# Optimization experiments

Hardware: AMD Instinct MI355X
Metric: run time of the kernel (lower is better)

The kernel has to match this reference:

```python
import jax, jax.numpy as jnp
import numpy as np

B = 256          # batch
H = 1024         # conditioning_size (dec_hid_dim)
D = 256          # gst_dim
G = 32           # num_gst
C = 16           # num_cells
O = 256          # output_size


def setup_inputs() -> dict:
    key = jax.random.key(0)
    ks = jax.random.split(key, 7)
    hidden = jax.random.normal(ks[0], (B, H), dtype=jnp.float32)
    # per-cell embedding tables: nn.Embedding(num_gst, gst_dim) stacked over cells
    gst_emb = jax.random.normal(ks[1], (C, G, D), dtype=jnp.float32)
    # per-cell Linear(gst_dim + cond, cond): weight [H, H + D] (torch [out, in]), bias [H]
    attn_w = jax.random.normal(ks[2], (C, H, H + D), dtype=jnp.float32) * 0.02
    attn_b = jax.random.normal(ks[3], (C, H), dtype=jnp.float32) * 0.02
    # per-cell v: Parameter(torch.rand(cond))
    v = jax.random.uniform(ks[4], (C, H), dtype=jnp.float32)
    # out Linear(gst_dim, output_size)
    out_w = jax.random.normal(ks[5], (O, D), dtype=jnp.float32) * 0.02
    out_b = jax.random.normal(ks[6], (O,), dtype=jnp.float32) * 0.02
    return {"hidden": hidden, "gst_emb": gst_emb, "attn_w": attn_w,
            "attn_b": attn_b, "v": v, "out_w": out_w, "out_b": out_b}


def reference(hidden, gst_emb, attn_w, attn_b, v, out_w, out_b):
    # Original concatenates (hidden, encoder_outputs) along features; split the
    # linear weight accordingly instead of materializing the concat.
    w_hid = attn_w[:, :, :H]        # [C, H, H]
    w_enc = attn_w[:, :, H:]        # [C, H, D]
    # embedding lookup of arange(G) == the table rows themselves (same for all batch)
    enc = gst_emb                   # [C, G, D]
    hid_part = jnp.einsum('bh,coh->bco', hidden, w_hid)     # [B, C, Ho]
    enc_part = jnp.einsum('cgd,cod->cgo', enc, w_enc)       # [C, G, Ho]
    energy = jnp.tanh(hid_part[:, :, None, :] + enc_part[None]
                      + attn_b[None, :, None, :])           # [B, C, G, Ho]
    scores = jnp.einsum('bcgh,ch->bcg', energy, v)          # [B, C, G]
    attention = jax.nn.softmax(scores, axis=-1)             # softmax over num_gst
    weighted = jnp.einsum('bcg,cgd->bcd', attention, enc)   # [B, C, D]
    att_cat = attention.reshape(B, C * G)                   # torch.cat(att_list, dim=1)
    pooled = jnp.mean(weighted, axis=1)                     # [B, D]
    out = pooled @ out_w.T + out_b                          # [B, O]
    return (att_cat, out)
```

## Files before the change

kernel.cpp:

```cpp
#include <hip/hip_runtime.h>
#include <hip/hip_bf16.h>

#define B_  256
#define H_  1024
#define D_  256
#define G_  32
#define C_  16
#define O_  256
#define HD_ 1280
#define N1_ 16384
#define RS_ 36

typedef __attribute__((ext_vector_type(8))) short short8;
typedef __attribute__((ext_vector_type(4))) short s16x4;
typedef __attribute__((ext_vector_type(4))) float f32x4;

#define MFMA16(a, b, c) __builtin_amdgcn_mfma_f32_16x16x32_bf16((a), (b), (c), 0, 0, 0)

__device__ __forceinline__ float tanh_c(float x) {
    float y = __expf(2.f * x);
    float t = 1.f - 2.f * __builtin_amdgcn_rcpf(y + 1.f);
    return fminf(fmaxf(t, -0.99999994f), 0.99999994f);
}

__device__ __forceinline__ short bfhi(float x) {
    return (short)(__float_as_uint(x) >> 16);
}
__device__ __forceinline__ short bflo(float x) {
    float fhi = __uint_as_float(__float_as_uint(x) & 0xFFFF0000u);
    return (short)(__float_as_uint(x - fhi) >> 16);
}

__device__ __forceinline__ void split4(const float4 v, s16x4& hi, s16x4& lo) {
    hi[0] = bfhi(v.x); lo[0] = bflo(v.x);
    hi[1] = bfhi(v.y); lo[1] = bflo(v.y);
    hi[2] = bfhi(v.z); lo[2] = bflo(v.z);
    hi[3] = bfhi(v.w); lo[3] = bflo(v.w);
}

__global__ __launch_bounds__(512) void gemm1_kernel(
    const float* __restrict__ hidden, const float* __restrict__ attn_w,
    const float* __restrict__ attn_b, float* __restrict__ hp)
{
    __shared__ short AsH[128 * RS_];
    __shared__ short AsL[128 * RS_];
    __shared__ short BsH[64 * RS_];
    __shared__ short BsL[64 * RS_];

    const int tid  = threadIdx.x;
    const int wave = tid >> 6, lane = tid & 63;
    const int m0 = blockIdx.x * 128;
    const int n0 = blockIdx.y * 64;
    const int wm = (wave >> 1) * 32;
    const int wn = (wave & 1) * 32;
    const int l16 = lane & 15;
    const int lk  = (lane >> 4) * 8;

    f32x4 acc[2][2];
    for (int mi = 0; mi < 2; ++mi)
        for (int ni = 0; ni < 2; ++ni)
            acc[mi][ni] = f32x4{0.f, 0.f, 0.f, 0.f};

    int rA[2], cA[2];
    #pragma unroll
    for (int i = 0; i < 2; ++i) {
        const int chunk = tid + i * 512;
        rA[i] = chunk >> 3;
        cA[i] = (chunk & 7) * 4;
    }
    const int rB = tid >> 3, cB = (tid & 7) * 4;

    const float* pA0 = hidden + rA[0] * H_ + m0 * H_ + cA[0];
    const float* pA1 = hidden + rA[1] * H_ + m0 * H_ + cA[1];
    const float* pB  = attn_w + (size_t)(n0 + rB) * HD_ + cB;

    float4 va[2], vb;
    va[0] = *(const float4*)(pA0);
    va[1] = *(const float4*)(pA1);
    vb    = *(const float4*)(pB);

    for (int k0 = 0; k0 < H_; k0 += 32) {
        __syncthreads();
        #pragma unroll
        for (int i = 0; i < 2; ++i) {
            s16x4 h, l;
            split4(va[i], h, l);
            *(s16x4*)(AsH + rA[i] * RS_ + cA[i]) = h;
            *(s16x4*)(AsL + rA[i] * RS_ + cA[i]) = l;
        }
        {
            s16x4 h, l;
            split4(vb, h, l);
            *(s16x4*)(BsH + rB * RS_ + cB) = h;
            *(s16x4*)(BsL + rB * RS_ + cB) = l;
        }
        __syncthreads();

        if (k0 + 32 < H_) {
            const int kn = k0 + 32;
            va[0] = *(const float4*)(pA0 + kn);
            va[1] = *(const float4*)(pA1 + kn);
            vb    = *(const float4*)(pB  + kn);
        }

        short8 ah[2], al[2], bh[2], bl[2];
        #pragma unroll
        for (int mi = 0; mi < 2; ++mi) {
            ah[mi] = *(const short8*)(AsH + (wm + mi * 16 + l16) * RS_ + lk);
            al[mi] = *(const short8*)(AsL + (wm + mi * 16 + l16) * RS_ + lk);
        }
        #pragma unroll
        for (int ni = 0; ni < 2; ++ni) {
            bh[ni] = *(const short8*)(BsH + (wn + ni * 16 + l16) * RS_ + lk);
            bl[ni] = *(const short8*)(BsL + (wn + ni * 16 + l16) * RS_ + lk);
        }
        #pragma unroll
        for (int mi = 0; mi < 2; ++mi)
            #pragma unroll
            for (int ni = 0; ni < 2; ++ni) {
                acc[mi][ni] = MFMA16(ah[mi], bh[ni], acc[mi][ni]);
                acc[mi][ni] = MFMA16(al[mi], bh[ni], acc[mi][ni]);
                acc[mi][ni] = MFMA16(ah[mi], bl[ni], acc[mi][ni]);
            }
    }

    const int lr = (lane >> 4) * 4;
    #pragma unroll
    for (int mi = 0; mi < 2; ++mi) {
        #pragma unroll
        for (int ni = 0; ni < 2; ++ni) {
            const int col  = n0 + wn + ni * 16 + l16;
            const float bias = attn_b[col];
            float* dst = hp + (size_t)(m0 + wm + mi * 16 + lr) * N1_ + col;
            f32x4 vacc = acc[mi][ni];
            dst[0]        = tanh_c(vacc[0] + bias);
            dst[N1_]      = tanh_c(vacc[1] + bias);
            dst[2 * N1_]  = tanh_c(vacc[2] + bias);
            dst[3 * N1_]  = tanh_c(vacc[3] + bias);
        }
    }
}

__global__ __launch_bounds__(256) void gemm2_kernel(
    const float* __restrict__ enc, const float* __restrict__ attn_w,
    float* __restrict__ ep)
{
    const int tid  = threadIdx.x;
    const int wave = tid >> 6, lane = tid & 63;
    const int c  = blockIdx.y;
    const int n0 = blockIdx.x * 64 + wave * 16;
    const int l16 = lane & 15;
    const int lk  = (lane >> 4) * 8;

    f32x4 acc[2];
    acc[0] = f32x4{0.f, 0.f, 0.f, 0.f};
    acc[1] = f32x4{0.f, 0.f, 0.f, 0.f};

    const float* encp = enc + c * (G_ * D_);
    const float* wp   = attn_w + (size_t)c * H_ * HD_ + H_;

    #pragma unroll
    for (int kk = 0; kk < 8; ++kk) {
        const int k0 = kk * 32 + lk;
        short8 ah[2], al[2], bh, bl;
        #pragma unroll
        for (int mi = 0; mi < 2; ++mi) {
            const float* p = encp + (mi * 16 + l16) * D_ + k0;
            s16x4 h0, l0, h1, l1;
            split4(*(const float4*)p, h0, l0);
            split4(*(const float4*)(p + 4), h1, l1);
            ah[mi] = short8{h0[0],h0[1],h0[2],h0[3],h1[0],h1[1],h1[2],h1[3]};
            al[mi] = short8{l0[0],l0[1],l0[2],l0[3],l1[0],l1[1],l1[2],l1[3]};
        }
        {
            const float* p = wp + (size_t)(n0 + l16) * HD_ + k0;
            s16x4 h0, l0, h1, l1;
            split4(*(const float4*)p, h0, l0);
            split4(*(const float4*)(p + 4), h1, l1);
            bh = short8{h0[0],h0[1],h0[2],h0[3],h1[0],h1[1],h1[2],h1[3]};
            bl = short8{l0[0],l0[1],l0[2],l0[3],l1[0],l1[1],l1[2],l1[3]};
        }
        #pragma unroll
        for (int mi = 0; mi < 2; ++mi) {
            acc[mi] = MFMA16(ah[mi], bh, acc[mi]);
            acc[mi] = MFMA16(al[mi], bh, acc[mi]);
            acc[mi] = MFMA16(ah[mi], bl, acc[mi]);
        }
    }

    const int lr = (lane >> 4) * 4;
    #pragma unroll
    for (int mi = 0; mi < 2; ++mi) {
        const int g = mi * 16 + lr;
        const int o = n0 + l16;
        float* dst = ep + (c * G_ + g) * H_ + o;
        f32x4 vacc = acc[mi];
        dst[0]      = tanh_c(vacc[0]);
        dst[H_]     = tanh_c(vacc[1]);
        dst[2 * H_] = tanh_c(vacc[2]);
        dst[3 * H_] = tanh_c(vacc[3]);
    }
}

__global__ __launch_bounds__(256) void attn_kernel(
    const float* __restrict__ hp, const float* __restrict__ ep,
    const float* __restrict__ v, const float* __restrict__ enc,
    float* __restrict__ out, float* __restrict__ wt)
{
    const int c = blockIdx.x, b = blockIdx.y;
    const int tid  = threadIdx.x;
    const int wave = tid >> 6, lane = tid & 63;

    __shared__ float s_att[G_];
    __shared__ float s_sc[G_];

    float tav[16], vv[16];
    const float* hprow = hp + (size_t)b * N1_ + c * H_;
    const float* vrow  = v + c * H_;
    #pragma unroll
    for (int j = 0; j < 16; ++j) {
        const int o = lane + j * 64;
        tav[j] = hprow[o];
        vv[j]  = vrow[o];
    }

    #pragma unroll
    for (int gg = 0; gg < 8; ++gg) {
        const int g = wave * 8 + gg;
        const float* eprow = ep + (c * G_ + g) * H_;
        float s = 0.f;
        #pragma unroll
        for (int j = 0; j < 16; ++j) {
            const float tb  = eprow[lane + j * 64];
            const float ta  = tav[j];
            const float num = ta + tb;
            const float den = fmaf(ta, tb, 1.f);
            const float t   = num * __builtin_amdgcn_rcpf(den);
            s = fmaf(t, vv[j], s);
        }
        #pragma unroll
        for (int off = 32; off > 0; off >>= 1)
            s += __shfl_down(s, off, 64);
        if (lane == 0) s_sc[g] = s;
    }
    __syncthreads();

    if (tid < 32) {
        float s = s_sc[tid];
        float m = s;
        #pragma unroll
        for (int off = 16; off > 0; off >>= 1)
            m = fmaxf(m, __shfl_xor(m, off, 32));
        const float e = __expf(s - m);
        float sum = e;
        #pragma unroll
        for (int off = 16; off > 0; off >>= 1)
            sum += __shfl_xor(sum, off, 32);
        const float a = e / sum;
        s_att[tid] = a;
        out[(size_t)b * (C_ * G_) + c * G_ + tid] = a;
    }
    __syncthreads();

    float wsum = 0.f;
    const float* encc = enc + c * (G_ * D_) + tid;
    #pragma unroll
    for (int g = 0; g < G_; ++g)
        wsum += s_att[g] * encc[g * D_];
    wt[(size_t)(b * C_ + c) * D_ + tid] = wsum;
}

__global__ __launch_bounds__(256) void out_kernel(
    const float* __restrict__ wt, const float* __restrict__ out_w,
    const float* __restrict__ out_b, float* __restrict__ out)
{
    const int b = blockIdx.x, tid = threadIdx.x;
    __shared__ float pooled[D_];

    float s = 0.f;
    #pragma unroll
    for (int c = 0; c < C_; ++c)
        s += wt[(size_t)(b * C_ + c) * D_ + tid];
    pooled[tid] = s * (1.f / 16.f);
    __syncthreads();

    float acc = out_b[tid];
    const float* wrow = out_w + tid * D_;
    #pragma unroll 8
    for (int dc = 0; dc < 64; ++dc) {
        float4 w4 = *(const float4*)(wrow + dc * 4);
        acc += pooled[dc * 4 + 0] * w4.x;
        acc += pooled[dc * 4 + 1] * w4.y;
        acc += pooled[dc * 4 + 2] * w4.z;
        acc += pooled[dc * 4 + 3] * w4.w;
    }
    out[(size_t)B_ * (C_ * G_) + b * O_ + tid] = acc;
}

extern "C" void kernel_launch(void* const* d_in, const int* in_sizes, int n_in,
                              void* d_out, int out_size, void* d_ws, size_t ws_size,
                              hipStream_t stream) {
    const float* hidden = (const float*)d_in[0];
    const float* enc    = (const float*)d_in[1];
    const float* attn_w = (const float*)d_in[2];
    const float* attn_b = (const float*)d_in[3];
    const float* v      = (const float*)d_in[4];
    const float* out_w  = (const float*)d_in[5];
    const float* out_b  = (const float*)d_in[6];
    float* out = (float*)d_out;

    float* hp = (float*)d_ws;
    float* ep = hp + (size_t)B_ * N1_;
    float* wt = ep + (size_t)C_ * G_ * H_;

    gemm1_kernel<<<dim3(2, 256), 512, 0, stream>>>(hidden, attn_w, attn_b, hp);
    gemm2_kernel<<<dim3(16, C_), 256, 0, stream>>>(enc, attn_w, ep);
    attn_kernel<<<dim3(C_, B_), 256, 0, stream>>>(hp, ep, v, enc, out, wt);
    out_kernel<<<B_, 256, 0, stream>>>(wt, out_w, out_b, out);
}
```

Before: 207.7 us.

## Enlarge gemm1 tile to 128x128 and batch four rows per attention block

gemm1 now computes 128x128 output tiles, with each wave handling 64x32 instead of 32x32. This halves the grid and raises the MFMA work per LDS fragment load. The attention kernel processes four batch rows per block, so each ep row and enc element loaded is reused four times, and the grid shrinks by four. In exchange there is more register pressure (acc[4][2], tav[4][16]) and fewer blocks to spread across CUs.

```diff
diff --git a/kernel.cpp b/kernel.cpp
--- a/kernel.cpp
+++ b/kernel.cpp
@@ -44,40 +44,43 @@
 {
     __shared__ short AsH[128 * RS_];
     __shared__ short AsL[128 * RS_];
-    __shared__ short BsH[64 * RS_];
-    __shared__ short BsL[64 * RS_];
+    __shared__ short BsH[128 * RS_];
+    __shared__ short BsL[128 * RS_];
 
     const int tid  = threadIdx.x;
     const int wave = tid >> 6, lane = tid & 63;
     const int m0 = blockIdx.x * 128;
-    const int n0 = blockIdx.y * 64;
-    const int wm = (wave >> 1) * 32;
-    const int wn = (wave & 1) * 32;
+    const int n0 = blockIdx.y * 128;
+    const int wm = (wave >> 2) * 64;
+    const int wn = (wave & 3) * 32;
     const int l16 = lane & 15;
     const int lk  = (lane >> 4) * 8;
 
-    f32x4 acc[2][2];
-    for (int mi = 0; mi < 2; ++mi)
+    f32x4 acc[4][2];
+    #pragma unroll
+    for (int mi = 0; mi < 4; ++mi)
+        #pragma unroll
         for (int ni = 0; ni < 2; ++ni)
             acc[mi][ni] = f32x4{0.f, 0.f, 0.f, 0.f};
 
-    int rA[2], cA[2];
+    int rr[2], cc[2];
     #pragma unroll
     for (int i = 0; i < 2; ++i) {
         const int chunk = tid + i * 512;
-        rA[i] = chunk >> 3;
-        cA[i] = (chunk & 7) * 4;
-    }
-    const int rB = tid >> 3, cB = (tid & 7) * 4;
-
-    const float* pA0 = hidden + rA[0] * H_ + m0 * H_ + cA[0];
-    const float* pA1 = hidden + rA[1] * H_ + m0 * H_ + cA[1];
-    const float* pB  = attn_w + (size_t)(n0 + rB) * HD_ + cB;
-
-    float4 va[2], vb;
+        rr[i] = chunk >> 3;
+        cc[i] = (chunk & 7) * 4;
+    }
+
+    const float* pA0 = hidden + (m0 + rr[0]) * H_ + cc[0];
+    const float* pA1 = hidden + (m0 + rr[1]) * H_ + cc[1];
+    const float* pB0 = attn_w + (size_t)(n0 + rr[0]) * HD_ + cc[0];
+    const float* pB1 = attn_w + (size_t)(n0 + rr[1]) * HD_ + cc[1];
+
+    float4 va[2], vb[2];
     va[0] = *(const float4*)(pA0);
     va[1] = *(const float4*)(pA1);
-    vb    = *(const float4*)(pB);
+    vb[0] = *(const float4*)(pB0);
+    vb[1] = *(const float4*)(pB1);
 
     for (int k0 = 0; k0 < H_; k0 += 32) {
         __syncthreads();
@@ -85,14 +88,11 @@
         for (int i = 0; i < 2; ++i) {
             s16x4 h, l;
             split4(va[i], h, l);
-            *(s16x4*)(AsH + rA[i] * RS_ + cA[i]) = h;
-            *(s16x4*)(AsL + rA[i] * RS_ + cA[i]) = l;
-        }
-        {
-            s16x4 h, l;
-            split4(vb, h, l);
-            *(s16x4*)(BsH + rB * RS_ + cB) = h;
-            *(s16x4*)(BsL + rB * RS_ + cB) = l;
+            *(s16x4*)(AsH + rr[i] * RS_ + cc[i]) = h;
+            *(s16x4*)(AsL + rr[i] * RS_ + cc[i]) = l;
+            split4(vb[i], h, l);
+            *(s16x4*)(BsH + rr[i] * RS_ + cc[i]) = h;
+            *(s16x4*)(BsL + rr[i] * RS_ + cc[i]) = l;
         }
         __syncthreads();
 
@@ -100,12 +100,13 @@
             const int kn = k0 + 32;
             va[0] = *(const float4*)(pA0 + kn);
             va[1] = *(const float4*)(pA1 + kn);
-            vb    = *(const float4*)(pB  + kn);
-        }
-
-        short8 ah[2], al[2], bh[2], bl[2];
-        #pragma unroll
-        for (int mi = 0; mi < 2; ++mi) {
+            vb[0] = *(const float4*)(pB0 + kn);
+            vb[1] = *(const float4*)(pB1 + kn);
+        }
+
+        short8 ah[4], al[4], bh[2], bl[2];
+        #pragma unroll
+        for (int mi = 0; mi < 4; ++mi) {
             ah[mi] = *(const short8*)(AsH + (wm + mi * 16 + l16) * RS_ + lk);
             al[mi] = *(const short8*)(AsL + (wm + mi * 16 + l16) * RS_ + lk);
         }
@@ -115,7 +116,7 @@
             bl[ni] = *(const short8*)(BsL + (wn + ni * 16 + l16) * RS_ + lk);
         }
         #pragma unroll
-        for (int mi = 0; mi < 2; ++mi)
+        for (int mi = 0; mi < 4; ++mi)
             #pragma unroll
             for (int ni = 0; ni < 2; ++ni) {
                 acc[mi][ni] = MFMA16(ah[mi], bh[ni], acc[mi][ni]);
@@ -126,7 +127,7 @@
 
     const int lr = (lane >> 4) * 4;
     #pragma unroll
-    for (int mi = 0; mi < 2; ++mi) {
+    for (int mi = 0; mi < 4; ++mi) {
         #pragma unroll
         for (int ni = 0; ni < 2; ++ni) {
             const int col  = n0 + wn + ni * 16 + l16;
@@ -207,46 +208,57 @@
     const float* __restrict__ v, const float* __restrict__ enc,
     float* __restrict__ out, float* __restrict__ wt)
 {
-    const int c = blockIdx.x, b = blockIdx.y;
+    const int c  = blockIdx.x;
+    const int b0 = blockIdx.y * 4;
     const int tid  = threadIdx.x;
     const int wave = tid >> 6, lane = tid & 63;
 
-    __shared__ float s_att[G_];
-    __shared__ float s_sc[G_];
-
-    float tav[16], vv[16];
-    const float* hprow = hp + (size_t)b * N1_ + c * H_;
-    const float* vrow  = v + c * H_;
+    __shared__ float s_att[4][G_];
+    __shared__ float s_sc[G_][4];
+
+    float tav[4][16], vv[16];
+    const float* vrow = v + c * H_;
     #pragma unroll
     for (int j = 0; j < 16; ++j) {
         const int o = lane + j * 64;
-        tav[j] = hprow[o];
-        vv[j]  = vrow[o];
+        vv[j] = vrow[o];
+        #pragma unroll
+        for (int bi = 0; bi < 4; ++bi)
+            tav[bi][j] = hp[(size_t)(b0 + bi) * N1_ + c * H_ + o];
     }
 
     #pragma unroll
     for (int gg = 0; gg < 8; ++gg) {
         const int g = wave * 8 + gg;
         const float* eprow = ep + (c * G_ + g) * H_;
-        float s = 0.f;
+        float s[4] = {0.f, 0.f, 0.f, 0.f};
         #pragma unroll
         for (int j = 0; j < 16; ++j) {
-            const float tb  = eprow[lane + j * 64];
-            const float ta  = tav[j];
-            const float num = ta + tb;
-            const float den = fmaf(ta, tb, 1.f);
-            const float t   = num * __builtin_amdgcn_rcpf(den);
-            s = fmaf(t, vv[j], s);
+            const float tb = eprow[lane + j * 64];
+            #pragma unroll
+            for (int bi = 0; bi < 4; ++bi) {
+                const float ta  = tav[bi][j];
+                const float den = fmaf(ta, tb, 1.f);
+                const float r   = __builtin_amdgcn_rcpf(den);
+                s[bi] = fmaf((ta + tb) * r, vv[j], s[bi]);
+            }
         }
         #pragma unroll
         for (int off = 32; off > 0; off >>= 1)
-            s += __shfl_down(s, off, 64);
-        if (lane == 0) s_sc[g] = s;
+            #pragma unroll
+            for (int bi = 0; bi < 4; ++bi)
+                s[bi] += __shfl_down(s[bi], off, 64);
+        if (lane == 0) {
+            #pragma unroll
+            for (int bi = 0; bi < 4; ++bi)
+                s_sc[g][bi] = s[bi];
+        }
     }
     __syncthreads();
 
-    if (tid < 32) {
-        float s = s_sc[tid];
+    if (tid < 128) {
+        const int bi = tid >> 5, gl = tid & 31;
+        float s = s_sc[gl][bi];
         float m = s;
         #pragma unroll
         for (int off = 16; off > 0; off >>= 1)
@@ -257,17 +269,23 @@
         for (int off = 16; off > 0; off >>= 1)
             sum += __shfl_xor(sum, off, 32);
         const float a = e / sum;
-        s_att[tid] = a;
-        out[(size_t)b * (C_ * G_) + c * G_ + tid] = a;
+        s_att[bi][gl] = a;
+        out[(size_t)(b0 + bi) * (C_ * G_) + c * G_ + gl] = a;
     }
     __syncthreads();
 
-    float wsum = 0.f;
+    float w[4] = {0.f, 0.f, 0.f, 0.f};
     const float* encc = enc + c * (G_ * D_) + tid;
     #pragma unroll
-    for (int g = 0; g < G_; ++g)
-        wsum += s_att[g] * encc[g * D_];
-    wt[(size_t)(b * C_ + c) * D_ + tid] = wsum;
+    for (int g = 0; g < G_; ++g) {
+        const float e = encc[g * D_];
+        #pragma unroll
+        for (int bi = 0; bi < 4; ++bi)
+            w[bi] = fmaf(s_att[bi][g], e, w[bi]);
+    }
+    #pragma unroll
+    for (int bi = 0; bi < 4; ++bi)
+        wt[(size_t)((b0 + bi) * C_ + c) * D_ + tid] = w[bi];
 }
 
 __global__ __launch_bounds__(256) void out_kernel(
@@ -313,8 +331,8 @@
     float* ep = hp + (size_t)B_ * N1_;
     float* wt = ep + (size_t)C_ * G_ * H_;
 
-    gemm1_kernel<<<dim3(2, 256), 512, 0, stream>>>(hidden, attn_w, attn_b, hp);
+    gemm1_kernel<<<dim3(2, 128), 512, 0, stream>>>(hidden, attn_w, attn_b, hp);
     gemm2_kernel<<<dim3(16, C_), 256, 0, stream>>>(enc, attn_w, ep);
-    attn_kernel<<<dim3(C_, B_), 256, 0, stream>>>(hp, ep, v, enc, out, wt);
+    attn_kernel<<<dim3(C_, B_ / 4), 256, 0, stream>>>(hp, ep, v, enc, out, wt);
     out_kernel<<<B_, 256, 0, stream>>>(wt, out_w, out_b, out);
 }
```

Result: no change. 208.1 us (+0.2%).
